# Kernel tuning notes

Measured on AMD Instinct MI355X. Metric: run time of the kernel, lower is better.

Reference implementation:

```python
import jax, jax.numpy as jnp
import numpy as np

BN_EPS = 1e-5


def setup_inputs() -> dict:
    key = jax.random.key(0)
    ks = jax.random.split(key, 6)
    B, C, N = 4, 256, 4096
    d = C // 4
    x = jax.random.normal(ks[0], (B, C, N), dtype=jnp.float32)
    # q_conv.weight tied to k_conv.weight -> single wq used for both
    wq = jax.random.normal(ks[1], (d, C), dtype=jnp.float32) * (1.0 / np.sqrt(C))
    wv = jax.random.normal(ks[2], (C, C), dtype=jnp.float32) * (1.0 / np.sqrt(C))
    bv = jax.random.normal(ks[3], (C,), dtype=jnp.float32) * 0.01
    wt = jax.random.normal(ks[4], (C, C), dtype=jnp.float32) * (1.0 / np.sqrt(C))
    bt = jax.random.normal(ks[5], (C,), dtype=jnp.float32) * 0.01
    gamma = jnp.ones((C,), dtype=jnp.float32)
    beta = jnp.zeros((C,), dtype=jnp.float32)
    return {"x": x, "wq": wq, "wv": wv, "bv": bv, "wt": wt, "bt": bt,
            "gamma": gamma, "beta": beta}


def reference(x, wq, wv, bv, wt, bt, gamma, beta):
    # x: [B, C, N]
    # 1x1 conv projections (weight-tied Q/K)
    x_q = jnp.einsum('dc,bcn->bnd', wq, x)            # [B, N, d]
    x_k = jnp.einsum('dc,bcn->bdn', wq, x)            # [B, d, N]
    x_v = jnp.einsum('oc,bcn->bon', wv, x) + bv[None, :, None]  # [B, C, N]

    energy = jnp.einsum('bnd,bdm->bnm', x_q, x_k)     # [B, N, N]
    attn = jax.nn.softmax(energy, axis=-1)            # row softmax
    # L1 column-normalize (offset-attention double normalization)
    attn = attn / (1e-9 + jnp.sum(attn, axis=1, keepdims=True))

    x_a = jnp.einsum('bcn,bnm->bcm', x_v, attn)       # [B, C, N]
    x_d = x - x_a

    t = jnp.einsum('oc,bcn->bon', wt, x_d) + bt[None, :, None]  # trans_conv
    # BatchNorm1d in training mode: batch stats over (B, N) per channel
    mean = jnp.mean(t, axis=(0, 2), keepdims=True)
    var = jnp.var(t, axis=(0, 2), keepdims=True)
    t_hat = (t - mean) * jax.lax.rsqrt(var + BN_EPS)
    x_r = jax.nn.relu(gamma[None, :, None] * t_hat + beta[None, :, None])
    return x + x_r
```

## Files before the change

kernel.cpp:

```cpp
#include <hip/hip_runtime.h>

#define BB 4
#define CC 256
#define NN 4096
#define DD 64

typedef _Float16 h8_t __attribute__((ext_vector_type(8)));
typedef _Float16 h4_t __attribute__((ext_vector_type(4)));
typedef float fx4 __attribute__((ext_vector_type(4)));

#define MFMA16(a, b, c) __builtin_amdgcn_mfma_f32_16x16x32_f16((a), (b), (c), 0, 0, 0)

__global__ __launch_bounds__(256) void k0_prep(
    const float* __restrict__ wq, const float* __restrict__ wv, const float* __restrict__ wt,
    _Float16* __restrict__ wqH, _Float16* __restrict__ wvH, _Float16* __restrict__ wtH,
    float* __restrict__ bnsum, float* __restrict__ bnsumsq) {
  int i = blockIdx.x * 256 + threadIdx.x;
  int stride = gridDim.x * 256;
  for (int j = i; j < DD * CC; j += stride) wqH[j] = (_Float16)wq[j];
  for (int j = i; j < CC * CC; j += stride) wvH[j] = (_Float16)wv[j];
  for (int j = i; j < CC * CC; j += stride) wtH[j] = (_Float16)wt[j];
  if (i < CC) { bnsum[i] = 0.f; bnsumsq[i] = 0.f; }
}

__global__ __launch_bounds__(256) void k1a_transpose(const float* __restrict__ x,
                                                     _Float16* __restrict__ xt) {
  __shared__ float tile[32][33];
  int b = blockIdx.z;
  int c0 = blockIdx.y * 32, n0 = blockIdx.x * 32;
  int t = threadIdx.x;
  int tn = t & 31, tc = t >> 5;
  const float* xb = x + (size_t)b * CC * NN;
#pragma unroll
  for (int i = 0; i < 4; i++) {
    int c = tc + i * 8;
    tile[c][tn] = xb[(size_t)(c0 + c) * NN + n0 + tn];
  }
  __syncthreads();
  _Float16* xtb = xt + (size_t)b * NN * CC;
#pragma unroll
  for (int i = 0; i < 4; i++) {
    int n = tc + i * 8;
    xtb[(size_t)(n0 + n) * CC + c0 + tn] = (_Float16)tile[tn][n];
  }
}

__global__ __launch_bounds__(256, 2) void k1b_proj(
    const _Float16* __restrict__ xt, const _Float16* __restrict__ wqH,
    const _Float16* __restrict__ wvH, const float* __restrict__ bv,
    _Float16* __restrict__ qh, _Float16* __restrict__ vh) {
  int L = blockIdx.x;
  int xcd = L & 7, j = L >> 3;
  int b = xcd >> 1;
  int nB = ((xcd & 1) * 64 + j) * 32;
  int w = threadIdx.x >> 6, lane = threadIdx.x & 63;
  int g = lane >> 4, q = lane & 15;
  int wsub = w & 1, h = w >> 1;
  int n = nB + wsub * 16 + q;
  const _Float16* xr = xt + ((size_t)b * NN + n) * CC;
  fx4 accQ[4] = {};
  fx4 accV[8] = {};
  for (int kt = 0; kt < 8; kt++) {
    h8_t bf = *(const h8_t*)(xr + kt * 32 + g * 8);
    if (h == 0) {
#pragma unroll
      for (int ot = 0; ot < 4; ot++) {
        h8_t a = *(const h8_t*)(wqH + (size_t)(ot * 16 + q) * CC + kt * 32 + g * 8);
        accQ[ot] = MFMA16(a, bf, accQ[ot]);
      }
    }
#pragma unroll
    for (int ot = 0; ot < 8; ot++) {
      int o16 = h * 8 + ot;
      h8_t a = *(const h8_t*)(wvH + (size_t)(o16 * 16 + q) * CC + kt * 32 + g * 8);
      accV[ot] = MFMA16(a, bf, accV[ot]);
    }
  }
  if (h == 0) {
    _Float16* qr = qh + ((size_t)b * NN + n) * DD;
#pragma unroll
    for (int ot = 0; ot < 4; ot++) {
      h4_t hq;
#pragma unroll
      for (int r = 0; r < 4; r++) hq[r] = (_Float16)accQ[ot][r];
      *(h4_t*)(qr + ot * 16 + g * 4) = hq;
    }
  }
#pragma unroll
  for (int ot = 0; ot < 8; ot++) {
#pragma unroll
    for (int r = 0; r < 4; r++) {
      int o = (h * 8 + ot) * 16 + g * 4 + r;
      vh[((size_t)b * CC + o) * NN + n] = (_Float16)(accV[ot][r] + bv[o]);
    }
  }
}

__global__ __launch_bounds__(512, 2) void k2_stats(
    const _Float16* __restrict__ qh, float* __restrict__ rowmax,
    float* __restrict__ rowsuminv) {
  __shared__ float redb[8][64];
  __shared__ float rmLDS[64];
  int L = blockIdx.x;
  int xcd = L & 7, j = L >> 3;
  int b = xcd >> 1;
  int mB = ((xcd & 1) * 32 + j) * 64;
  int w = threadIdx.x >> 6, lane = threadIdx.x & 63;
  int g = lane >> 4, q = lane & 15;
  const _Float16* qb = qh + (size_t)b * NN * DD;
  h8_t aq[4][2];
#pragma unroll
  for (int mt = 0; mt < 4; mt++) {
    aq[mt][0] = *(const h8_t*)(qb + (size_t)(mB + mt * 16 + q) * DD + g * 8);
    aq[mt][1] = *(const h8_t*)(qb + (size_t)(mB + mt * 16 + q) * DD + 32 + g * 8);
  }
  fx4 rmax[4];
#pragma unroll
  for (int mt = 0; mt < 4; mt++)
#pragma unroll
    for (int r = 0; r < 4; r++) rmax[mt][r] = -1e30f;
  for (int ch = 0; ch < 32; ch++) {
    int n0 = ch * 128 + w * 16;
    h8_t b0 = *(const h8_t*)(qb + (size_t)(n0 + q) * DD + g * 8);
    h8_t b1 = *(const h8_t*)(qb + (size_t)(n0 + q) * DD + 32 + g * 8);
#pragma unroll
    for (int mt = 0; mt < 4; mt++) {
      fx4 e = {};
      e = MFMA16(aq[mt][0], b0, e);
      e = MFMA16(aq[mt][1], b1, e);
#pragma unroll
      for (int r = 0; r < 4; r++) rmax[mt][r] = fmaxf(rmax[mt][r], e[r]);
    }
  }
#pragma unroll
  for (int off = 1; off < 16; off <<= 1)
#pragma unroll
    for (int mt = 0; mt < 4; mt++)
#pragma unroll
      for (int r = 0; r < 4; r++)
        rmax[mt][r] = fmaxf(rmax[mt][r], __shfl_xor(rmax[mt][r], off));
  if (q == 0) {
#pragma unroll
    for (int mt = 0; mt < 4; mt++)
#pragma unroll
      for (int r = 0; r < 4; r++) redb[w][mt * 16 + g * 4 + r] = rmax[mt][r];
  }
  __syncthreads();
  if (threadIdx.x < 64) {
    float M = redb[0][threadIdx.x];
#pragma unroll
    for (int w2 = 1; w2 < 8; w2++) M = fmaxf(M, redb[w2][threadIdx.x]);
    rmLDS[threadIdx.x] = M;
    rowmax[b * NN + mB + threadIdx.x] = M;
  }
  __syncthreads();
  float rmv[4][4];
#pragma unroll
  for (int mt = 0; mt < 4; mt++)
#pragma unroll
    for (int r = 0; r < 4; r++) rmv[mt][r] = rmLDS[mt * 16 + g * 4 + r];
  fx4 s[4] = {};
  for (int ch = 0; ch < 32; ch++) {
    int n0 = ch * 128 + w * 16;
    h8_t b0 = *(const h8_t*)(qb + (size_t)(n0 + q) * DD + g * 8);
    h8_t b1 = *(const h8_t*)(qb + (size_t)(n0 + q) * DD + 32 + g * 8);
#pragma unroll
    for (int mt = 0; mt < 4; mt++) {
      fx4 e = {};
      e = MFMA16(aq[mt][0], b0, e);
      e = MFMA16(aq[mt][1], b1, e);
#pragma unroll
      for (int r = 0; r < 4; r++) s[mt][r] += __expf(e[r] - rmv[mt][r]);
    }
  }
#pragma unroll
  for (int off = 1; off < 16; off <<= 1)
#pragma unroll
    for (int mt = 0; mt < 4; mt++)
#pragma unroll
      for (int r = 0; r < 4; r++) s[mt][r] += __shfl_xor(s[mt][r], off);
  if (q == 0) {
#pragma unroll
    for (int mt = 0; mt < 4; mt++)
#pragma unroll
      for (int r = 0; r < 4; r++) redb[w][mt * 16 + g * 4 + r] = s[mt][r];
  }
  __syncthreads();
  if (threadIdx.x < 64) {
    float S = redb[0][threadIdx.x];
#pragma unroll
    for (int w2 = 1; w2 < 8; w2++) S += redb[w2][threadIdx.x];
    rowsuminv[b * NN + mB + threadIdx.x] = 1.f / S;
  }
}

__global__ __launch_bounds__(512, 2) void k3_colsum(
    const _Float16* __restrict__ qh, const float* __restrict__ rowmax,
    const float* __restrict__ rowsuminv, float* __restrict__ colsum) {
  __shared__ float redb[8][64];
  int L = blockIdx.x;
  int xcd = L & 7, j = L >> 3;
  int b = xcd >> 1;
  int mB = ((xcd & 1) * 32 + j) * 64;
  int w = threadIdx.x >> 6, lane = threadIdx.x & 63;
  int g = lane >> 4, q = lane & 15;
  const _Float16* qb = qh + (size_t)b * NN * DD;
  const float* rm = rowmax + b * NN;
  const float* ri = rowsuminv + b * NN;
  h8_t aq[4][2];
#pragma unroll
  for (int mt = 0; mt < 4; mt++) {
    aq[mt][0] = *(const h8_t*)(qb + (size_t)(mB + mt * 16 + q) * DD + g * 8);
    aq[mt][1] = *(const h8_t*)(qb + (size_t)(mB + mt * 16 + q) * DD + 32 + g * 8);
  }
  fx4 colp[4] = {};
  for (int ch = 0; ch < 32; ch++) {
    int n0 = ch * 128 + w * 16;
    h8_t b0 = *(const h8_t*)(qb + (size_t)(n0 + q) * DD + g * 8);
    h8_t b1 = *(const h8_t*)(qb + (size_t)(n0 + q) * DD + 32 + g * 8);
    float rmn = rm[n0 + q];
    float rin = ri[n0 + q];
#pragma unroll
    for (int mt = 0; mt < 4; mt++) {
      fx4 e = {};
      e = MFMA16(aq[mt][0], b0, e);
      e = MFMA16(aq[mt][1], b1, e);
#pragma unroll
      for (int r = 0; r < 4; r++) colp[mt][r] += __expf(e[r] - rmn) * rin;
    }
  }
#pragma unroll
  for (int off = 1; off < 16; off <<= 1)
#pragma unroll
    for (int mt = 0; mt < 4; mt++)
#pragma unroll
      for (int r = 0; r < 4; r++) colp[mt][r] += __shfl_xor(colp[mt][r], off);
  if (q == 0) {
#pragma unroll
    for (int mt = 0; mt < 4; mt++)
#pragma unroll
      for (int r = 0; r < 4; r++) redb[w][mt * 16 + g * 4 + r] = colp[mt][r];
  }
  __syncthreads();
  if (threadIdx.x < 64) {
    float S = redb[0][threadIdx.x];
#pragma unroll
    for (int w2 = 1; w2 < 8; w2++) S += redb[w2][threadIdx.x];
    colsum[b * NN + mB + threadIdx.x] = S;
  }
}

__global__ __launch_bounds__(512, 2) void k4_main(
    const _Float16* __restrict__ qh, const _Float16* __restrict__ vh,
    const _Float16* __restrict__ wtH, const float* __restrict__ rowmax,
    const float* __restrict__ rowsuminv, const float* __restrict__ colsum,
    const float* __restrict__ x, const float* __restrict__ bt,
    _Float16* __restrict__ th, float* __restrict__ bnsum, float* __restrict__ bnsumsq) {
  __shared__ _Float16 Pb[2][64 * 128];
  __shared__ _Float16 xdT[64 * 256];
  int L = blockIdx.x;
  int xcd = L & 7, jj = L >> 3;
  int b = xcd >> 1;
  int mB = ((xcd & 1) * 32 + jj) * 64;
  int w = threadIdx.x >> 6, lane = threadIdx.x & 63;
  int g = lane >> 4, q = lane & 15;
  const _Float16* qb = qh + (size_t)b * NN * DD;
  const float* rm = rowmax + b * NN;
  const float* ri = rowsuminv + b * NN;

  h8_t aq[4][2];
#pragma unroll
  for (int mt = 0; mt < 4; mt++) {
    aq[mt][0] = *(const h8_t*)(qb + (size_t)(mB + mt * 16 + q) * DD + g * 8);
    aq[mt][1] = *(const h8_t*)(qb + (size_t)(mB + mt * 16 + q) * DD + 32 + g * 8);
  }

  {
    int n0 = 0 * 128 + w * 16;
    h8_t b0 = *(const h8_t*)(qb + (size_t)(n0 + q) * DD + g * 8);
    h8_t b1 = *(const h8_t*)(qb + (size_t)(n0 + q) * DD + 32 + g * 8);
    float rmn = rm[n0 + q], rin = ri[n0 + q];
    int nl = w * 16 + q;
#pragma unroll
    for (int mt = 0; mt < 4; mt++) {
      fx4 e = {};
      e = MFMA16(aq[mt][0], b0, e);
      e = MFMA16(aq[mt][1], b1, e);
#pragma unroll
      for (int r = 0; r < 4; r++) {
        int m = mt * 16 + 4 * g + r;
        Pb[0][(m * 128 + nl) ^ ((m & 7) << 3)] = (_Float16)(__expf(e[r] - rmn) * rin);
      }
    }
  }
  __syncthreads();

  fx4 acc[2][4] = {};
  int swzq = (q & 7) << 3;
  for (int ch = 0; ch < 32; ch++) {
    int cur = ch & 1;
    int nB = ch * 128;
    h8_t b0n, b1n;
    float rmn = 0.f, rin = 0.f;
    if (ch < 31) {
      int n0 = (ch + 1) * 128 + w * 16;
      b0n = *(const h8_t*)(qb + (size_t)(n0 + q) * DD + g * 8);
      b1n = *(const h8_t*)(qb + (size_t)(n0 + q) * DD + 32 + g * 8);
      rmn = rm[n0 + q];
      rin = ri[n0 + q];
    }
#pragma unroll
    for (int kt = 0; kt < 4; kt++) {
      h8_t bp[4];
#pragma unroll
      for (int mt = 0; mt < 4; mt++) {
        int m = mt * 16 + q;
        bp[mt] = *(const h8_t*)&Pb[cur][(m * 128 + kt * 32 + g * 8) ^ swzq];
      }
#pragma unroll
      for (int ct = 0; ct < 2; ct++) {
        h8_t av = *(const h8_t*)(vh + ((size_t)b * CC + 32 * w + ct * 16 + q) * NN + nB + kt * 32 + g * 8);
#pragma unroll
        for (int mt = 0; mt < 4; mt++)
          acc[ct][mt] = MFMA16(av, bp[mt], acc[ct][mt]);
      }
    }
    if (ch < 31) {
      int nl = w * 16 + q;
#pragma unroll
      for (int mt = 0; mt < 4; mt++) {
        fx4 e = {};
        e = MFMA16(aq[mt][0], b0n, e);
        e = MFMA16(aq[mt][1], b1n, e);
#pragma unroll
        for (int r = 0; r < 4; r++) {
          int m = mt * 16 + 4 * g + r;
          Pb[cur ^ 1][(m * 128 + nl) ^ ((m & 7) << 3)] = (_Float16)(__expf(e[r] - rmn) * rin);
        }
      }
    }
    __syncthreads();
  }

  float cinv[4];
#pragma unroll
  for (int mt = 0; mt < 4; mt++)
    cinv[mt] = 1.f / (1e-9f + colsum[b * NN + mB + mt * 16 + q]);
#pragma unroll
  for (int ct = 0; ct < 2; ct++) {
#pragma unroll
    for (int mt = 0; mt < 4; mt++) {
      h4_t hd;
#pragma unroll
      for (int r = 0; r < 4; r++) {
        int c = 32 * w + ct * 16 + g * 4 + r;
        int m = mB + mt * 16 + q;
        float xa = acc[ct][mt][r] * cinv[mt];
        float xd = x[((size_t)b * CC + c) * NN + m] - xa;
        hd[r] = (_Float16)xd;
      }
      int mloc = mt * 16 + q;
      int c0 = 32 * w + ct * 16 + g * 4;
      *(h4_t*)&xdT[(mloc * 256 + c0) ^ ((mloc & 7) << 3)] = hd;
    }
  }
  __syncthreads();
  fx4 acct[2][4] = {};
  for (int kt = 0; kt < 8; kt++) {
    h8_t bx[4];
#pragma unroll
    for (int mt = 0; mt < 4; mt++) {
      int m = mt * 16 + q;
      bx[mt] = *(const h8_t*)&xdT[(m * 256 + kt * 32 + g * 8) ^ swzq];
    }
#pragma unroll
    for (int ot = 0; ot < 2; ot++) {
      h8_t a = *(const h8_t*)(wtH + (size_t)(32 * w + ot * 16 + q) * CC + kt * 32 + g * 8);
#pragma unroll
      for (int mt = 0; mt < 4; mt++)
        acct[ot][mt] = MFMA16(a, bx[mt], acct[ot][mt]);
    }
  }
#pragma unroll
  for (int ot = 0; ot < 2; ot++) {
#pragma unroll
    for (int r = 0; r < 4; r++) {
      int o = 32 * w + ot * 16 + g * 4 + r;
      float btv = bt[o];
      float s1 = 0.f, s2 = 0.f;
#pragma unroll
      for (int mt = 0; mt < 4; mt++) {
        float tv = acct[ot][mt][r] + btv;
        th[((size_t)b * CC + o) * NN + mB + mt * 16 + q] = (_Float16)tv;
        s1 += tv;
        s2 += tv * tv;
      }
#pragma unroll
      for (int off = 1; off < 16; off <<= 1) {
        s1 += __shfl_xor(s1, off);
        s2 += __shfl_xor(s2, off);
      }
      if (q == 0) {
        atomicAdd(&bnsum[o], s1);
        atomicAdd(&bnsumsq[o], s2);
      }
    }
  }
}

__global__ __launch_bounds__(256) void k5_bnfinal(
    const float* __restrict__ bnsum, const float* __restrict__ bnsumsq,
    const float* __restrict__ gamma, const float* __restrict__ beta,
    float* __restrict__ bnsc, float* __restrict__ bnsh) {
  int c = threadIdx.x;
  float inv = 1.f / (float)(BB * NN);
  float mean = bnsum[c] * inv;
  float var = bnsumsq[c] * inv - mean * mean;
  float sc = gamma[c] * rsqrtf(var + 1e-5f);
  bnsc[c] = sc;
  bnsh[c] = beta[c] - mean * sc;
}

__global__ __launch_bounds__(256) void k6_final(
    const float* __restrict__ x, const _Float16* __restrict__ th,
    const float* __restrict__ bnsc, const float* __restrict__ bnsh,
    float* __restrict__ out) {
  size_t i = (size_t)blockIdx.x * 256 + threadIdx.x;
  size_t base = i * 8;
  int c = (int)((base >> 12) & 255);
  h8_t t8 = *(const h8_t*)(th + base);
  float sc = bnsc[c], sh = bnsh[c];
  fx4 x0 = *(const fx4*)(x + base);
  fx4 x1 = *(const fx4*)(x + base + 4);
  fx4 o0, o1;
#pragma unroll
  for (int j2 = 0; j2 < 4; j2++) {
    o0[j2] = x0[j2] + fmaxf(0.f, sc * (float)t8[j2] + sh);
    o1[j2] = x1[j2] + fmaxf(0.f, sc * (float)t8[j2 + 4] + sh);
  }
  *(fx4*)(out + base) = o0;
  *(fx4*)(out + base + 4) = o1;
}

extern "C" void kernel_launch(void* const* d_in, const int* in_sizes, int n_in,
                              void* d_out, int out_size, void* d_ws, size_t ws_size,
                              hipStream_t stream) {
  const float* x = (const float*)d_in[0];
  const float* wq = (const float*)d_in[1];
  const float* wv = (const float*)d_in[2];
  const float* bv = (const float*)d_in[3];
  const float* wt = (const float*)d_in[4];
  const float* bt = (const float*)d_in[5];
  const float* gamma = (const float*)d_in[6];
  const float* beta = (const float*)d_in[7];
  char* ws = (char*)d_ws;
  _Float16* qh = (_Float16*)(ws + 0);
  _Float16* vh = (_Float16*)(ws + 2097152);
  _Float16* xt = (_Float16*)(ws + 10485760);
  _Float16* wqH = (_Float16*)(ws + 18874368);
  _Float16* wvH = (_Float16*)(ws + 18907136);
  _Float16* wtH = (_Float16*)(ws + 19038208);
  float* rowmax = (float*)(ws + 19169280);
  float* rowsuminv = (float*)(ws + 19234816);
  float* colsum = (float*)(ws + 19300352);
  float* bnsum = (float*)(ws + 19365888);
  float* bnsumsq = (float*)(ws + 19366912);
  float* bnsc = (float*)(ws + 19367936);
  float* bnsh = (float*)(ws + 19368960);
  _Float16* th = (_Float16*)(ws + 19369984);

  hipLaunchKernelGGL(k0_prep, dim3(64), dim3(256), 0, stream,
                     wq, wv, wt, wqH, wvH, wtH, bnsum, bnsumsq);
  hipLaunchKernelGGL(k1a_transpose, dim3(128, 8, 4), dim3(256), 0, stream, x, xt);
  hipLaunchKernelGGL(k1b_proj, dim3(512), dim3(256), 0, stream, xt, wqH, wvH, bv, qh, vh);
  hipLaunchKernelGGL(k2_stats, dim3(256), dim3(512), 0, stream, qh, rowmax, rowsuminv);
  hipLaunchKernelGGL(k3_colsum, dim3(256), dim3(512), 0, stream, qh, rowmax, rowsuminv, colsum);
  hipLaunchKernelGGL(k4_main, dim3(256), dim3(512), 0, stream, qh, vh, wtH,
                     rowmax, rowsuminv, colsum, x, bt, th, bnsum, bnsumsq);
  hipLaunchKernelGGL(k5_bnfinal, dim3(1), dim3(256), 0, stream,
                     bnsum, bnsumsq, gamma, beta, bnsc, bnsh);
  hipLaunchKernelGGL(k6_final, dim3(2048), dim3(256), 0, stream,
                     x, th, bnsc, bnsh, (float*)d_out);
}
```

Measured before the change: 305.0 us.

## Fuse column-sum pass into main attention kernel and halve per-block row tile

Drops the separate column-sum kernel (a full recompute of QK^T and exp). Column sums are now accumulated while the P tile is built inside the main kernel and applied after the PV product, which is valid because the normalization is per output column. Row tiles shrink from 64 to 32 with twice as many blocks and higher occupancy. The kernel also uses padded LDS strides instead of XOR swizzle, register-prefetches V and K, reads x from the transposed fp16 copy, and folds the BN finalize into the last kernel. The cost is per-element recomputation of the BN scale, extra fp16 rounding of x, and less reuse per block.

Result: slower. 376.1 us (+23.3%).

```diff
diff --git a/kernel.cpp b/kernel.cpp
--- a/kernel.cpp
+++ b/kernel.cpp
@@ -96,27 +96,28 @@
   }
 }
 
-__global__ __launch_bounds__(512, 2) void k2_stats(
+__global__ __launch_bounds__(512, 4) void k2_stats(
     const _Float16* __restrict__ qh, float* __restrict__ rowmax,
     float* __restrict__ rowsuminv) {
-  __shared__ float redb[8][64];
-  __shared__ float rmLDS[64];
+  __shared__ float redb[8][32];
+  __shared__ float rmS[32];
   int L = blockIdx.x;
-  int xcd = L & 7, j = L >> 3;
+  int xcd = L & 7;
   int b = xcd >> 1;
-  int mB = ((xcd & 1) * 32 + j) * 64;
+  int mi = (L & 1) * 64 + (L >> 3);
+  int mB = mi * 32;
   int w = threadIdx.x >> 6, lane = threadIdx.x & 63;
   int g = lane >> 4, q = lane & 15;
   const _Float16* qb = qh + (size_t)b * NN * DD;
-  h8_t aq[4][2];
-#pragma unroll
-  for (int mt = 0; mt < 4; mt++) {
+  h8_t aq[2][2];
+#pragma unroll
+  for (int mt = 0; mt < 2; mt++) {
     aq[mt][0] = *(const h8_t*)(qb + (size_t)(mB + mt * 16 + q) * DD + g * 8);
     aq[mt][1] = *(const h8_t*)(qb + (size_t)(mB + mt * 16 + q) * DD + 32 + g * 8);
   }
-  fx4 rmax[4];
-#pragma unroll
-  for (int mt = 0; mt < 4; mt++)
+  fx4 rmax[2];
+#pragma unroll
+  for (int mt = 0; mt < 2; mt++)
 #pragma unroll
     for (int r = 0; r < 4; r++) rmax[mt][r] = -1e30f;
   for (int ch = 0; ch < 32; ch++) {
@@ -124,7 +125,7 @@
     h8_t b0 = *(const h8_t*)(qb + (size_t)(n0 + q) * DD + g * 8);
     h8_t b1 = *(const h8_t*)(qb + (size_t)(n0 + q) * DD + 32 + g * 8);
 #pragma unroll
-    for (int mt = 0; mt < 4; mt++) {
+    for (int mt = 0; mt < 2; mt++) {
       fx4 e = {};
       e = MFMA16(aq[mt][0], b0, e);
       e = MFMA16(aq[mt][1], b1, e);
@@ -135,37 +136,37 @@
 #pragma unroll
   for (int off = 1; off < 16; off <<= 1)
 #pragma unroll
-    for (int mt = 0; mt < 4; mt++)
+    for (int mt = 0; mt < 2; mt++)
 #pragma unroll
       for (int r = 0; r < 4; r++)
         rmax[mt][r] = fmaxf(rmax[mt][r], __shfl_xor(rmax[mt][r], off));
   if (q == 0) {
 #pragma unroll
-    for (int mt = 0; mt < 4; mt++)
+    for (int mt = 0; mt < 2; mt++)
 #pragma unroll
       for (int r = 0; r < 4; r++) redb[w][mt * 16 + g * 4 + r] = rmax[mt][r];
   }
   __syncthreads();
-  if (threadIdx.x < 64) {
+  if (threadIdx.x < 32) {
     float M = redb[0][threadIdx.x];
 #pragma unroll
     for (int w2 = 1; w2 < 8; w2++) M = fmaxf(M, redb[w2][threadIdx.x]);
-    rmLDS[threadIdx.x] = M;
+    rmS[threadIdx.x] = M;
     rowmax[b * NN + mB + threadIdx.x] = M;
   }
   __syncthreads();
-  float rmv[4][4];
-#pragma unroll
-  for (int mt = 0; mt < 4; mt++)
-#pragma unroll
-    for (int r = 0; r < 4; r++) rmv[mt][r] = rmLDS[mt * 16 + g * 4 + r];
-  fx4 s[4] = {};
+  float rmv[2][4];
+#pragma unroll
+  for (int mt = 0; mt < 2; mt++)
+#pragma unroll
+    for (int r = 0; r < 4; r++) rmv[mt][r] = rmS[mt * 16 + g * 4 + r];
+  fx4 s[2] = {};
   for (int ch = 0; ch < 32; ch++) {
     int n0 = ch * 128 + w * 16;
     h8_t b0 = *(const h8_t*)(qb + (size_t)(n0 + q) * DD + g * 8);
     h8_t b1 = *(const h8_t*)(qb + (size_t)(n0 + q) * DD + 32 + g * 8);
 #pragma unroll
-    for (int mt = 0; mt < 4; mt++) {
+    for (int mt = 0; mt < 2; mt++) {
       fx4 e = {};
       e = MFMA16(aq[mt][0], b0, e);
       e = MFMA16(aq[mt][1], b1, e);
@@ -176,17 +177,17 @@
 #pragma unroll
   for (int off = 1; off < 16; off <<= 1)
 #pragma unroll
-    for (int mt = 0; mt < 4; mt++)
+    for (int mt = 0; mt < 2; mt++)
 #pragma unroll
       for (int r = 0; r < 4; r++) s[mt][r] += __shfl_xor(s[mt][r], off);
   if (q == 0) {
 #pragma unroll
-    for (int mt = 0; mt < 4; mt++)
+    for (int mt = 0; mt < 2; mt++)
 #pragma unroll
       for (int r = 0; r < 4; r++) redb[w][mt * 16 + g * 4 + r] = s[mt][r];
   }
   __syncthreads();
-  if (threadIdx.x < 64) {
+  if (threadIdx.x < 32) {
     float S = redb[0][threadIdx.x];
 #pragma unroll
     for (int w2 = 1; w2 < 8; w2++) S += redb[w2][threadIdx.x];
@@ -194,207 +195,162 @@
   }
 }
 
-__global__ __launch_bounds__(512, 2) void k3_colsum(
-    const _Float16* __restrict__ qh, const float* __restrict__ rowmax,
-    const float* __restrict__ rowsuminv, float* __restrict__ colsum) {
-  __shared__ float redb[8][64];
+#define PSTR 264
+__global__ __launch_bounds__(512, 4) void k4_main(
+    const _Float16* __restrict__ qh, const _Float16* __restrict__ vh,
+    const _Float16* __restrict__ wtH, const float* __restrict__ rowmax,
+    const float* __restrict__ rowsuminv, const _Float16* __restrict__ xt,
+    const float* __restrict__ bt, _Float16* __restrict__ th,
+    float* __restrict__ bnsum, float* __restrict__ bnsumsq) {
+  __shared__ _Float16 Pb[2][32 * PSTR];
+  __shared__ _Float16 xdT[32 * PSTR];
+  __shared__ float csLDS[8][32];
+  __shared__ float csT[32];
   int L = blockIdx.x;
-  int xcd = L & 7, j = L >> 3;
+  int xcd = L & 7;
   int b = xcd >> 1;
-  int mB = ((xcd & 1) * 32 + j) * 64;
+  int mi = (L & 1) * 64 + (L >> 3);
+  int mB = mi * 32;
   int w = threadIdx.x >> 6, lane = threadIdx.x & 63;
   int g = lane >> 4, q = lane & 15;
   const _Float16* qb = qh + (size_t)b * NN * DD;
+  const _Float16* vb = vh + (size_t)b * CC * NN;
   const float* rm = rowmax + b * NN;
   const float* ri = rowsuminv + b * NN;
-  h8_t aq[4][2];
-#pragma unroll
-  for (int mt = 0; mt < 4; mt++) {
+
+  h8_t aq[2][2];
+#pragma unroll
+  for (int mt = 0; mt < 2; mt++) {
     aq[mt][0] = *(const h8_t*)(qb + (size_t)(mB + mt * 16 + q) * DD + g * 8);
     aq[mt][1] = *(const h8_t*)(qb + (size_t)(mB + mt * 16 + q) * DD + 32 + g * 8);
   }
-  fx4 colp[4] = {};
-  for (int ch = 0; ch < 32; ch++) {
-    int n0 = ch * 128 + w * 16;
-    h8_t b0 = *(const h8_t*)(qb + (size_t)(n0 + q) * DD + g * 8);
-    h8_t b1 = *(const h8_t*)(qb + (size_t)(n0 + q) * DD + 32 + g * 8);
-    float rmn = rm[n0 + q];
-    float rin = ri[n0 + q];
-#pragma unroll
-    for (int mt = 0; mt < 4; mt++) {
-      fx4 e = {};
-      e = MFMA16(aq[mt][0], b0, e);
-      e = MFMA16(aq[mt][1], b1, e);
-#pragma unroll
-      for (int r = 0; r < 4; r++) colp[mt][r] += __expf(e[r] - rmn) * rin;
-    }
-  }
-#pragma unroll
-  for (int off = 1; off < 16; off <<= 1)
-#pragma unroll
-    for (int mt = 0; mt < 4; mt++)
-#pragma unroll
-      for (int r = 0; r < 4; r++) colp[mt][r] += __shfl_xor(colp[mt][r], off);
-  if (q == 0) {
-#pragma unroll
-    for (int mt = 0; mt < 4; mt++)
-#pragma unroll
-      for (int r = 0; r < 4; r++) redb[w][mt * 16 + g * 4 + r] = colp[mt][r];
-  }
-  __syncthreads();
-  if (threadIdx.x < 64) {
-    float S = redb[0][threadIdx.x];
-#pragma unroll
-    for (int w2 = 1; w2 < 8; w2++) S += redb[w2][threadIdx.x];
-    colsum[b * NN + mB + threadIdx.x] = S;
-  }
-}
-
-__global__ __launch_bounds__(512, 2) void k4_main(
-    const _Float16* __restrict__ qh, const _Float16* __restrict__ vh,
-    const _Float16* __restrict__ wtH, const float* __restrict__ rowmax,
-    const float* __restrict__ rowsuminv, const float* __restrict__ colsum,
-    const float* __restrict__ x, const float* __restrict__ bt,
-    _Float16* __restrict__ th, float* __restrict__ bnsum, float* __restrict__ bnsumsq) {
-  __shared__ _Float16 Pb[2][64 * 128];
-  __shared__ _Float16 xdT[64 * 256];
-  int L = blockIdx.x;
-  int xcd = L & 7, jj = L >> 3;
-  int b = xcd >> 1;
-  int mB = ((xcd & 1) * 32 + jj) * 64;
-  int w = threadIdx.x >> 6, lane = threadIdx.x & 63;
-  int g = lane >> 4, q = lane & 15;
-  const _Float16* qb = qh + (size_t)b * NN * DD;
-  const float* rm = rowmax + b * NN;
-  const float* ri = rowsuminv + b * NN;
-
-  h8_t aq[4][2];
-#pragma unroll
-  for (int mt = 0; mt < 4; mt++) {
-    aq[mt][0] = *(const h8_t*)(qb + (size_t)(mB + mt * 16 + q) * DD + g * 8);
-    aq[mt][1] = *(const h8_t*)(qb + (size_t)(mB + mt * 16 + q) * DD + 32 + g * 8);
-  }
-
-  {
-    int n0 = 0 * 128 + w * 16;
-    h8_t b0 = *(const h8_t*)(qb + (size_t)(n0 + q) * DD + g * 8);
-    h8_t b1 = *(const h8_t*)(qb + (size_t)(n0 + q) * DD + 32 + g * 8);
-    float rmn = rm[n0 + q], rin = ri[n0 + q];
-    int nl = w * 16 + q;
-#pragma unroll
-    for (int mt = 0; mt < 4; mt++) {
-      fx4 e = {};
-      e = MFMA16(aq[mt][0], b0, e);
-      e = MFMA16(aq[mt][1], b1, e);
+
+  float csum[2] = {0.f, 0.f};
+  h8_t pa0[2], pa1[2];
+
+  auto loadK = [&](int ph) {
+#pragma unroll
+    for (int sc = 0; sc < 2; sc++) {
+      int n0 = ph * 256 + sc * 128 + w * 16;
+      pa0[sc] = *(const h8_t*)(qb + (size_t)(n0 + q) * DD + g * 8);
+      pa1[sc] = *(const h8_t*)(qb + (size_t)(n0 + q) * DD + 32 + g * 8);
+    }
+  };
+  auto buildP = [&](int ph, int nb) {
+#pragma unroll
+    for (int sc = 0; sc < 2; sc++) {
+      int n0 = ph * 256 + sc * 128 + w * 16;
+      fx4 rmv = *(const fx4*)(rm + n0 + 4 * g);
+      fx4 riv = *(const fx4*)(ri + n0 + 4 * g);
+#pragma unroll
+      for (int mt = 0; mt < 2; mt++) {
+        fx4 e = {};
+        e = MFMA16(pa0[sc], aq[mt][0], e);
+        e = MFMA16(pa1[sc], aq[mt][1], e);
+        h4_t p;
+        float sacc = 0.f;
+#pragma unroll
+        for (int r = 0; r < 4; r++) {
+          float pv = __expf(e[r] - rmv[r]) * riv[r];
+          p[r] = (_Float16)pv;
+          sacc += pv;
+        }
+        csum[mt] += sacc;
+        *(h4_t*)&Pb[nb][(mt * 16 + q) * PSTR + sc * 128 + w * 16 + 4 * g] = p;
+      }
+    }
+  };
+
+  loadK(0);
+  buildP(0, 0);
+  loadK(1);
+  __syncthreads();
+
+  fx4 acc[2][2] = {};
+  for (int ph = 0; ph < 16; ph++) {
+    int cur = ph & 1;
+    const _Float16* vr0 = vb + (size_t)(32 * w + q) * NN + ph * 256;
+    const _Float16* vr1 = vb + (size_t)(32 * w + 16 + q) * NN + ph * 256;
+    h8_t av0[4], av1[4];
+#pragma unroll
+    for (int p0 = 0; p0 < 4; p0++) {
+      av0[p0] = *(const h8_t*)(vr0 + p0 * 32 + g * 8);
+      av1[p0] = *(const h8_t*)(vr1 + p0 * 32 + g * 8);
+    }
+    if (ph < 15) buildP(ph + 1, cur ^ 1);
+    if (ph < 14) loadK(ph + 2);
+#pragma unroll
+    for (int kt = 0; kt < 8; kt++) {
+      int pp = kt & 3;
+      h8_t bp0 = *(const h8_t*)&Pb[cur][q * PSTR + kt * 32 + g * 8];
+      h8_t bp1 = *(const h8_t*)&Pb[cur][(16 + q) * PSTR + kt * 32 + g * 8];
+      acc[0][0] = MFMA16(av0[pp], bp0, acc[0][0]);
+      acc[0][1] = MFMA16(av0[pp], bp1, acc[0][1]);
+      acc[1][0] = MFMA16(av1[pp], bp0, acc[1][0]);
+      acc[1][1] = MFMA16(av1[pp], bp1, acc[1][1]);
+      if (kt < 4) {
+        av0[pp] = *(const h8_t*)(vr0 + (kt + 4) * 32 + g * 8);
+        av1[pp] = *(const h8_t*)(vr1 + (kt + 4) * 32 + g * 8);
+      }
+    }
+    __syncthreads();
+  }
+
+#pragma unroll
+  for (int mt = 0; mt < 2; mt++) {
+    float cs = csum[mt];
+    cs += __shfl_xor(cs, 16);
+    cs += __shfl_xor(cs, 32);
+    if (lane < 16) csLDS[w][mt * 16 + q] = cs;
+  }
+  __syncthreads();
+  if (threadIdx.x < 32) {
+    float s = 0.f;
+#pragma unroll
+    for (int w2 = 0; w2 < 8; w2++) s += csLDS[w2][threadIdx.x];
+    csT[threadIdx.x] = 1.f / (1e-9f + s);
+  }
+  __syncthreads();
+  float cinv[2] = {csT[q], csT[16 + q]};
+
+#pragma unroll
+  for (int ct = 0; ct < 2; ct++) {
+#pragma unroll
+    for (int mt = 0; mt < 2; mt++) {
+      h4_t xv = *(const h4_t*)(xt + ((size_t)b * NN + mB + mt * 16 + q) * CC + 32 * w + ct * 16 + 4 * g);
+      h4_t hd;
 #pragma unroll
       for (int r = 0; r < 4; r++) {
-        int m = mt * 16 + 4 * g + r;
-        Pb[0][(m * 128 + nl) ^ ((m & 7) << 3)] = (_Float16)(__expf(e[r] - rmn) * rin);
-      }
-    }
-  }
-  __syncthreads();
-
-  fx4 acc[2][4] = {};
-  int swzq = (q & 7) << 3;
-  for (int ch = 0; ch < 32; ch++) {
-    int cur = ch & 1;
-    int nB = ch * 128;
-    h8_t b0n, b1n;
-    float rmn = 0.f, rin = 0.f;
-    if (ch < 31) {
-      int n0 = (ch + 1) * 128 + w * 16;
-      b0n = *(const h8_t*)(qb + (size_t)(n0 + q) * DD + g * 8);
-      b1n = *(const h8_t*)(qb + (size_t)(n0 + q) * DD + 32 + g * 8);
-      rmn = rm[n0 + q];
-      rin = ri[n0 + q];
-    }
-#pragma unroll
-    for (int kt = 0; kt < 4; kt++) {
-      h8_t bp[4];
-#pragma unroll
-      for (int mt = 0; mt < 4; mt++) {
-        int m = mt * 16 + q;
-        bp[mt] = *(const h8_t*)&Pb[cur][(m * 128 + kt * 32 + g * 8) ^ swzq];
-      }
-#pragma unroll
-      for (int ct = 0; ct < 2; ct++) {
-        h8_t av = *(const h8_t*)(vh + ((size_t)b * CC + 32 * w + ct * 16 + q) * NN + nB + kt * 32 + g * 8);
-#pragma unroll
-        for (int mt = 0; mt < 4; mt++)
-          acc[ct][mt] = MFMA16(av, bp[mt], acc[ct][mt]);
-      }
-    }
-    if (ch < 31) {
-      int nl = w * 16 + q;
-#pragma unroll
-      for (int mt = 0; mt < 4; mt++) {
-        fx4 e = {};
-        e = MFMA16(aq[mt][0], b0n, e);
-        e = MFMA16(aq[mt][1], b1n, e);
-#pragma unroll
-        for (int r = 0; r < 4; r++) {
-          int m = mt * 16 + 4 * g + r;
-          Pb[cur ^ 1][(m * 128 + nl) ^ ((m & 7) << 3)] = (_Float16)(__expf(e[r] - rmn) * rin);
-        }
-      }
-    }
-    __syncthreads();
-  }
-
-  float cinv[4];
-#pragma unroll
-  for (int mt = 0; mt < 4; mt++)
-    cinv[mt] = 1.f / (1e-9f + colsum[b * NN + mB + mt * 16 + q]);
-#pragma unroll
-  for (int ct = 0; ct < 2; ct++) {
-#pragma unroll
-    for (int mt = 0; mt < 4; mt++) {
-      h4_t hd;
-#pragma unroll
-      for (int r = 0; r < 4; r++) {
-        int c = 32 * w + ct * 16 + g * 4 + r;
-        int m = mB + mt * 16 + q;
-        float xa = acc[ct][mt][r] * cinv[mt];
-        float xd = x[((size_t)b * CC + c) * NN + m] - xa;
+        float xd = (float)xv[r] - acc[ct][mt][r] * cinv[mt];
         hd[r] = (_Float16)xd;
       }
-      int mloc = mt * 16 + q;
-      int c0 = 32 * w + ct * 16 + g * 4;
-      *(h4_t*)&xdT[(mloc * 256 + c0) ^ ((mloc & 7) << 3)] = hd;
-    }
-  }
-  __syncthreads();
-  fx4 acct[2][4] = {};
+      *(h4_t*)&xdT[(mt * 16 + q) * PSTR + 32 * w + ct * 16 + 4 * g] = hd;
+    }
+  }
+  __syncthreads();
+
+  fx4 acct[2][2] = {};
   for (int kt = 0; kt < 8; kt++) {
-    h8_t bx[4];
-#pragma unroll
-    for (int mt = 0; mt < 4; mt++) {
-      int m = mt * 16 + q;
-      bx[mt] = *(const h8_t*)&xdT[(m * 256 + kt * 32 + g * 8) ^ swzq];
-    }
+    h8_t bx0 = *(const h8_t*)&xdT[q * PSTR + kt * 32 + g * 8];
+    h8_t bx1 = *(const h8_t*)&xdT[(16 + q) * PSTR + kt * 32 + g * 8];
 #pragma unroll
     for (int ot = 0; ot < 2; ot++) {
       h8_t a = *(const h8_t*)(wtH + (size_t)(32 * w + ot * 16 + q) * CC + kt * 32 + g * 8);
-#pragma unroll
-      for (int mt = 0; mt < 4; mt++)
-        acct[ot][mt] = MFMA16(a, bx[mt], acct[ot][mt]);
+      acct[ot][0] = MFMA16(a, bx0, acct[ot][0]);
+      acct[ot][1] = MFMA16(a, bx1, acct[ot][1]);
     }
   }
 #pragma unroll
   for (int ot = 0; ot < 2; ot++) {
 #pragma unroll
     for (int r = 0; r < 4; r++) {
-      int o = 32 * w + ot * 16 + g * 4 + r;
+      int o = 32 * w + ot * 16 + 4 * g + r;
       float btv = bt[o];
-      float s1 = 0.f, s2 = 0.f;
-#pragma unroll
-      for (int mt = 0; mt < 4; mt++) {
-        float tv = acct[ot][mt][r] + btv;
-        th[((size_t)b * CC + o) * NN + mB + mt * 16 + q] = (_Float16)tv;
-        s1 += tv;
-        s2 += tv * tv;
-      }
+      float t0 = acct[ot][0][r] + btv;
+      float t1 = acct[ot][1][r] + btv;
+      th[((size_t)b * CC + o) * NN + mB + q] = (_Float16)t0;
+      th[((size_t)b * CC + o) * NN + mB + 16 + q] = (_Float16)t1;
+      float s1 = t0 + t1, s2 = t0 * t0 + t1 * t1;
 #pragma unroll
       for (int off = 1; off < 16; off <<= 1) {
         s1 += __shfl_xor(s1, off);
@@ -408,28 +364,20 @@
   }
 }
 
-__global__ __launch_bounds__(256) void k5_bnfinal(
+__global__ __launch_bounds__(256) void k6_final(
+    const float* __restrict__ x, const _Float16* __restrict__ th,
     const float* __restrict__ bnsum, const float* __restrict__ bnsumsq,
     const float* __restrict__ gamma, const float* __restrict__ beta,
-    float* __restrict__ bnsc, float* __restrict__ bnsh) {
-  int c = threadIdx.x;
+    float* __restrict__ out) {
+  size_t i = (size_t)blockIdx.x * 256 + threadIdx.x;
+  size_t base = i * 8;
+  int c = (int)((base >> 12) & 255);
   float inv = 1.f / (float)(BB * NN);
   float mean = bnsum[c] * inv;
   float var = bnsumsq[c] * inv - mean * mean;
   float sc = gamma[c] * rsqrtf(var + 1e-5f);
-  bnsc[c] = sc;
-  bnsh[c] = beta[c] - mean * sc;
-}
-
-__global__ __launch_bounds__(256) void k6_final(
-    const float* __restrict__ x, const _Float16* __restrict__ th,
-    const float* __restrict__ bnsc, const float* __restrict__ bnsh,
-    float* __restrict__ out) {
-  size_t i = (size_t)blockIdx.x * 256 + threadIdx.x;
-  size_t base = i * 8;
-  int c = (int)((base >> 12) & 255);
+  float sh = beta[c] - mean * sc;
   h8_t t8 = *(const h8_t*)(th + base);
-  float sc = bnsc[c], sh = bnsh[c];
   fx4 x0 = *(const fx4*)(x + base);
   fx4 x1 = *(const fx4*)(x + base + 4);
   fx4 o0, o1;
@@ -462,23 +410,17 @@
   _Float16* wtH = (_Float16*)(ws + 19038208);
   float* rowmax = (float*)(ws + 19169280);
   float* rowsuminv = (float*)(ws + 19234816);
-  float* colsum = (float*)(ws + 19300352);
   float* bnsum = (float*)(ws + 19365888);
   float* bnsumsq = (float*)(ws + 19366912);
-  float* bnsc = (float*)(ws + 19367936);
-  float* bnsh = (float*)(ws + 19368960);
   _Float16* th = (_Float16*)(ws + 19369984);
 
   hipLaunchKernelGGL(k0_prep, dim3(64), dim3(256), 0, stream,
                      wq, wv, wt, wqH, wvH, wtH, bnsum, bnsumsq);
   hipLaunchKernelGGL(k1a_transpose, dim3(128, 8, 4), dim3(256), 0, stream, x, xt);
   hipLaunchKernelGGL(k1b_proj, dim3(512), dim3(256), 0, stream, xt, wqH, wvH, bv, qh, vh);
-  hipLaunchKernelGGL(k2_stats, dim3(256), dim3(512), 0, stream, qh, rowmax, rowsuminv);
-  hipLaunchKernelGGL(k3_colsum, dim3(256), dim3(512), 0, stream, qh, rowmax, rowsuminv, colsum);
-  hipLaunchKernelGGL(k4_main, dim3(256), dim3(512), 0, stream, qh, vh, wtH,
-                     rowmax, rowsuminv, colsum, x, bt, th, bnsum, bnsumsq);
-  hipLaunchKernelGGL(k5_bnfinal, dim3(1), dim3(256), 0, stream,
-                     bnsum, bnsumsq, gamma, beta, bnsc, bnsh);
+  hipLaunchKernelGGL(k2_stats, dim3(512), dim3(512), 0, stream, qh, rowmax, rowsuminv);
+  hipLaunchKernelGGL(k4_main, dim3(512), dim3(512), 0, stream, qh, vh, wtH,
+                     rowmax, rowsuminv, xt, bt, th, bnsum, bnsumsq);
   hipLaunchKernelGGL(k6_final, dim3(2048), dim3(256), 0, stream,
-                     x, th, bnsc, bnsh, (float*)d_out);
-}
+                     x, th, bnsum, bnsumsq, gamma, beta, (float*)d_out);
+}
```
